# Kernel tuning notes

Measured on AMD Instinct MI355X. Metric: run time of the kernel, lower is better.

Reference implementation:

```python
import jax, jax.numpy as jnp
import numpy as np

K = 8192
D = 512
BETA = 0.25


def setup_inputs() -> dict:
    key = jax.random.key(0)
    k_z, k_cb = jax.random.split(key)
    z = jax.random.normal(k_z, (8, 4096, D), dtype=jnp.float32)
    codebook = jax.random.normal(k_cb, (K, D), dtype=jnp.float32)
    return {"z": z, "codebook": codebook}


def reference(z, codebook):
    B, Q, Din = z.shape
    flat = z.reshape(-1, Din)                      # (N, D)
    x2 = jnp.sum(flat * flat, axis=1, keepdims=True)   # (N, 1)
    e2 = jnp.sum(codebook * codebook, axis=1)          # (K,)
    xe = flat @ codebook.T                             # (N, K)
    distances = x2 - 2.0 * xe + e2[None, :]
    indices = jnp.argmin(distances, axis=1)            # (N,)
    z_q = codebook[indices].reshape(B, Q, Din)

    codebook_loss = jnp.mean((z_q - jax.lax.stop_gradient(z)) ** 2)
    commitment_loss = jnp.mean((z - jax.lax.stop_gradient(z_q)) ** 2)
    vq_loss = codebook_loss + BETA * commitment_loss
    z_q_ste = z + jax.lax.stop_gradient(z_q - z)

    # perplexity from one-hot usage counts of this batch
    N = flat.shape[0]
    counts = jnp.zeros((codebook.shape[0],), dtype=jnp.float32).at[indices].add(1.0)
    probs = counts / jnp.asarray(N, dtype=jnp.float32)
    perplexity = jnp.exp(-jnp.sum(probs * jnp.log(probs + 1e-10)))

    return z_q_ste, vq_loss, indices.reshape(B, Q), perplexity
```

## Files before the change

kernel.cpp:

```cpp
#include <hip/hip_runtime.h>
#include <hip/hip_bf16.h>

#define K_CODES 8192
#define DIM     512
#define N_VEC   32768
#define MARGIN  0.35f

typedef __attribute__((ext_vector_type(8))) short   short8;
typedef __attribute__((ext_vector_type(8))) unsigned short ushort8;
typedef __attribute__((ext_vector_type(4))) float   float4x;

__device__ inline void gl_lds16(const void* g, void* l) {
    __builtin_amdgcn_global_load_lds(
        (const __attribute__((address_space(1))) unsigned int*)g,
        (__attribute__((address_space(3))) unsigned int*)l, 16, 0, 0);
}

__device__ inline unsigned short f2bf(float f) {
    unsigned int u = __float_as_uint(f);
    return (unsigned short)((u + 0x7FFFu + ((u >> 16) & 1u)) >> 16);
}

__global__ __launch_bounds__(256) void vq_prep(
    const float* __restrict__ z, const float* __restrict__ cb,
    float* __restrict__ x2, float* __restrict__ hne2,
    unsigned short* __restrict__ zh, unsigned short* __restrict__ ch) {
    int wave = threadIdx.x >> 6;
    int lane = threadIdx.x & 63;
    int row  = blockIdx.x * 4 + wave;
    bool isZ = row < N_VEC;
    int lr = isZ ? row : row - N_VEC;
    const float* src = isZ ? z + (size_t)row * DIM : cb + (size_t)lr * DIM;

    const float4* s4 = (const float4*)src;
    float4 v0 = s4[lane * 2];
    float4 v1 = s4[lane * 2 + 1];
    float f[8] = {v0.x, v0.y, v0.z, v0.w, v1.x, v1.y, v1.z, v1.w};

    float s = 0.0f;
    ushort8 h8;
#pragma unroll
    for (int i = 0; i < 8; ++i) { s += f[i] * f[i]; h8[i] = f2bf(f[i]); }
    ((ushort8*)(isZ ? zh : ch))[(size_t)lr * 64 + lane] = h8;

#pragma unroll
    for (int off = 32; off >= 1; off >>= 1) s += __shfl_xor(s, off, 64);
    if (lane == 0) {
        if (isZ) x2[lr] = s;
        else     hne2[lr] = -0.5f * s;
    }
}

__global__ __launch_bounds__(256, 2) void vq_gemm(
    const unsigned short* __restrict__ zh, const unsigned short* __restrict__ ch,
    const float* __restrict__ hne2,
    float* __restrict__ pG, int* __restrict__ pN, float* __restrict__ pG2) {
    __shared__ short8 AsC[1024];
    __shared__ short8 BsC[2048];

    const int tid  = threadIdx.x;
    const int w    = tid >> 6;
    const int lane = tid & 63;
    const int wM   = w & 1;
    const int wN   = w >> 1;
    const int rowBase   = blockIdx.x * 128;
    const int half      = blockIdx.y;
    const int codeBase0 = half * 4096;

    const int low3 = lane & 7, m15 = lane & 15, hi4 = lane >> 4;

    unsigned aOff[4];
#pragma unroll
    for (int i = 0; i < 4; ++i) {
        int cell = (w * 4 + i) * 64 + lane;
        int r = cell >> 3, qs = cell & 7, q = qs ^ (r & 7);
        aOff[i] = ((unsigned)(rowBase + r) * DIM + q * 8) * 2;
    }
    unsigned bOff[8];
#pragma unroll
    for (int i = 0; i < 8; ++i) {
        int cell = (w * 8 + i) * 64 + lane;
        int c = cell >> 3, qs = cell & 7, q = qs ^ (c & 7);
        bOff[i] = ((unsigned)c * DIM + q * 8) * 2;
    }

    int rIdx[4], cIdx[8];
#pragma unroll
    for (int mf = 0; mf < 4; ++mf) rIdx[mf] = (wM * 64 + mf * 16 + m15) * 8;
#pragma unroll
    for (int nf = 0; nf < 8; ++nf) cIdx[nf] = (wN * 128 + nf * 16 + m15) * 8;

    float g1[4][4], g2[4][4];
    int   n1[4][4];
#pragma unroll
    for (int mf = 0; mf < 4; ++mf)
#pragma unroll
        for (int rg = 0; rg < 4; ++rg) {
            g1[mf][rg] = -3.4e38f; g2[mf][rg] = -3.4e38f; n1[mf][rg] = 0;
        }

    const char* pA = (const char*)zh;
    for (int ct = 0; ct < 16; ++ct) {
        const int codeBase = codeBase0 + ct * 256;
        const char* pB = (const char*)ch + (size_t)codeBase * (DIM * 2);
        float4x acc[4][8];
#pragma unroll
        for (int mf = 0; mf < 4; ++mf)
#pragma unroll
            for (int nf = 0; nf < 8; ++nf) acc[mf][nf] = (float4x){0.f, 0.f, 0.f, 0.f};

        for (int dc = 0; dc < DIM; dc += 64) {
            const int dc2 = dc * 2;
            __syncthreads();
#pragma unroll
            for (int i = 0; i < 4; ++i)
                gl_lds16(pA + aOff[i] + dc2, &AsC[(w * 4 + i) * 64]);
#pragma unroll
            for (int i = 0; i < 8; ++i)
                gl_lds16(pB + bOff[i] + dc2, &BsC[(w * 8 + i) * 64]);
            __syncthreads();

#pragma unroll
            for (int ks = 0; ks < 2; ++ks) {
                const int qx = (ks * 4 + hi4) ^ low3;
                short8 a[4];
#pragma unroll
                for (int mf = 0; mf < 4; ++mf) a[mf] = AsC[rIdx[mf] + qx];
#pragma unroll
                for (int nf = 0; nf < 8; ++nf) {
                    short8 b = BsC[cIdx[nf] + qx];
#pragma unroll
                    for (int mf = 0; mf < 4; ++mf)
                        acc[mf][nf] = __builtin_amdgcn_mfma_f32_16x16x32_bf16(
                            a[mf], b, acc[mf][nf], 0, 0, 0);
                }
            }
        }

#pragma unroll
        for (int nf = 0; nf < 8; ++nf) {
            int nb = codeBase + wN * 128 + nf * 16 + m15;
            float hv = hne2[nb];
#pragma unroll
            for (int mf = 0; mf < 4; ++mf) {
#pragma unroll
                for (int rg = 0; rg < 4; ++rg) {
                    float g = acc[mf][nf][rg] + hv;
                    if (g > g1[mf][rg]) {
                        g2[mf][rg] = g1[mf][rg];
                        g1[mf][rg] = g; n1[mf][rg] = nb;
                    } else {
                        g2[mf][rg] = fmaxf(g2[mf][rg], g);
                    }
                }
            }
        }
    }

#pragma unroll
    for (int mf = 0; mf < 4; ++mf)
#pragma unroll
        for (int rg = 0; rg < 4; ++rg) {
            float a1 = g1[mf][rg], a2 = g2[mf][rg];
            int   an = n1[mf][rg];
#pragma unroll
            for (int off = 1; off <= 8; off <<= 1) {
                float b1 = __shfl_xor(a1, off, 64);
                int   bn = __shfl_xor(an, off, 64);
                float b2 = __shfl_xor(a2, off, 64);
                if (b1 > a1 || (b1 == a1 && bn < an)) {
                    a2 = fmaxf(a1, b2); a1 = b1; an = bn;
                } else {
                    a2 = fmaxf(a2, b1);
                }
            }
            if (m15 == 0) {
                int row  = rowBase + wM * 64 + mf * 16 + hi4 * 4 + rg;
                int slot = half * 2 + wN;
                pG [slot * N_VEC + row] = a1;
                pN [slot * N_VEC + row] = an;
                pG2[slot * N_VEC + row] = a2;
            }
        }
}

__global__ __launch_bounds__(256) void vq_scan(
    float* __restrict__ pG, const int* __restrict__ pN,
    const float* __restrict__ pG2,
    int* __restrict__ provIdx, int* __restrict__ flags,
    unsigned long long* __restrict__ keys,
    int* __restrict__ rescueRows, int* __restrict__ rescueCnt) {
    int r = blockIdx.x * 256 + threadIdx.x;
    float g1 = pG[r], g2 = pG2[r];
    int   n1 = pN[r];
#pragma unroll
    for (int s = 1; s < 4; ++s) {
        float a1 = pG [s * N_VEC + r];
        int   an = pN [s * N_VEC + r];
        float a2 = pG2[s * N_VEC + r];
        if (a1 > g1 || (a1 == g1 && an < n1)) {
            g2 = fmaxf(g1, a2); g1 = a1; n1 = an;
        } else {
            g2 = fmaxf(g2, a1);
        }
    }
    provIdx[r] = n1;
    pG[r] = g1;
    int fl = (g1 - g2 < MARGIN) ? 1 : 0;
    flags[r] = fl;
    if (fl) {
        keys[r] = ~0ull;
        int p = atomicAdd(rescueCnt, 1);
        rescueRows[p] = r;
    }
}

#define RBM 64
#define RBK 256
#define RBD 32

__global__ __launch_bounds__(256, 2) void vq_rescue(
    const float* __restrict__ z, const float* __restrict__ cb,
    const float* __restrict__ hne2,
    const int* __restrict__ rescueRows, const int* __restrict__ rescueCnt,
    unsigned long long* __restrict__ keys) {
    __shared__ float As[RBD][RBM];
    __shared__ float Bs[RBD][RBK];
    __shared__ int   rowOf[RBM];

    const int tid = threadIdx.x;
    const int tx  = tid & 31;
    const int ty  = tid >> 5;
    const int cnt = *rescueCnt;
    const int codeBase0 = blockIdx.y * 512;
    const int sw = (tx & 8) ? 4 : 0;
    const int sRow = tid >> 2;
    const int sQ   = tid & 3;

    for (int rt = blockIdx.x; rt * RBM < cnt; rt += gridDim.x) {
        const int slotBase = rt * RBM;
        __syncthreads();
        if (tid < RBM) rowOf[tid] = rescueRows[slotBase + tid];
        __syncthreads();

        float best[8];
        int   bidx[8];
#pragma unroll
        for (int i = 0; i < 8; ++i) { best[i] = 3.4e38f; bidx[i] = K_CODES; }

        for (int kt = 0; kt < 2; ++kt) {
            const int codeBase = codeBase0 + kt * RBK;
            float acc[8][8];
#pragma unroll
            for (int i = 0; i < 8; ++i)
#pragma unroll
                for (int j = 0; j < 8; ++j) acc[i][j] = 0.0f;

            for (int dc = 0; dc < DIM; dc += RBD) {
                __syncthreads();
                {
                    const float* srcA = z + (size_t)rowOf[sRow] * DIM + dc + sQ * 8;
                    float4 va0 = ((const float4*)srcA)[0];
                    float4 va1 = ((const float4*)srcA)[1];
                    int c0 = sQ * 8;
                    As[c0 + 0][sRow] = va0.x; As[c0 + 1][sRow] = va0.y;
                    As[c0 + 2][sRow] = va0.z; As[c0 + 3][sRow] = va0.w;
                    As[c0 + 4][sRow] = va1.x; As[c0 + 5][sRow] = va1.y;
                    As[c0 + 6][sRow] = va1.z; As[c0 + 7][sRow] = va1.w;
                }
                {
                    const float4* srcB = (const float4*)(cb + (size_t)(codeBase + tid) * DIM + dc);
#pragma unroll
                    for (int j = 0; j < 8; ++j) {
                        float4 v = srcB[j];
                        Bs[j * 4 + 0][tid] = v.x; Bs[j * 4 + 1][tid] = v.y;
                        Bs[j * 4 + 2][tid] = v.z; Bs[j * 4 + 3][tid] = v.w;
                    }
                }
                __syncthreads();

#pragma unroll
                for (int d = 0; d < RBD; ++d) {
                    float a[8], b[8];
                    *(float4*)&a[0] = *(const float4*)&As[d][ty * 8];
                    *(float4*)&a[4] = *(const float4*)&As[d][ty * 8 + 4];
                    *(float4*)&b[0] = *(const float4*)&Bs[d][tx * 8 + sw];
                    *(float4*)&b[4] = *(const float4*)&Bs[d][tx * 8 + (sw ^ 4)];
#pragma unroll
                    for (int i = 0; i < 8; ++i)
#pragma unroll
                        for (int j = 0; j < 8; ++j) acc[i][j] += a[i] * b[j];
                }
            }

#pragma unroll
            for (int j = 0; j < 8; ++j) {
                int code = codeBase + tx * 8 + ((j < 4) ? (sw + j) : ((sw ^ 4) + j - 4));
                float ev = -hne2[code];
#pragma unroll
                for (int i = 0; i < 8; ++i) {
                    float kv = ev - acc[i][j];
                    if (kv < best[i] || (kv == best[i] && code < bidx[i])) {
                        best[i] = kv;
                        bidx[i] = code;
                    }
                }
            }
        }

#pragma unroll
        for (int off = 16; off >= 1; off >>= 1) {
#pragma unroll
            for (int i = 0; i < 8; ++i) {
                float od = __shfl_xor(best[i], off, 64);
                int   oi = __shfl_xor(bidx[i], off, 64);
                if (od < best[i] || (od == best[i] && oi < bidx[i])) {
                    best[i] = od;
                    bidx[i] = oi;
                }
            }
        }

        if (tx == 0) {
#pragma unroll
            for (int i = 0; i < 8; ++i) {
                int slot = slotBase + ty * 8 + i;
                if (slot < cnt) {
                    unsigned long long key =
                        ((unsigned long long)__float_as_uint(best[i]) << 32) |
                        (unsigned long long)(unsigned)bidx[i];
                    atomicMin(&keys[rowOf[ty * 8 + i]], key);
                }
            }
        }
    }
}

__global__ __launch_bounds__(256) void vq_final(
    const float* __restrict__ gBest, const int* __restrict__ provIdx,
    const int* __restrict__ flags, const unsigned long long* __restrict__ keys,
    const float* __restrict__ x2, const float* __restrict__ cb,
    float* __restrict__ zq, float* __restrict__ idxf,
    float* __restrict__ counts, float* __restrict__ lossAcc) {
    __shared__ int   sIdx[256];
    __shared__ float wsum[4];
    const int tid = threadIdx.x;
    const int r   = blockIdx.x * 256 + tid;

    int n; float dist;
    if (flags[r]) {
        unsigned long long k = keys[r];
        n = (int)(unsigned)(k & 0xffffffffu);
        float kv = __uint_as_float((unsigned)(k >> 32));
        dist = x2[r] + 2.0f * kv;
    } else {
        n = provIdx[r];
        dist = x2[r] - 2.0f * gBest[r];
    }
    sIdx[tid] = n;
    idxf[r]   = (float)n;
    atomicAdd(&counts[n], 1.0f);

    float ls = dist;
#pragma unroll
    for (int off = 32; off >= 1; off >>= 1) ls += __shfl_xor(ls, off, 64);
    if ((tid & 63) == 0) wsum[tid >> 6] = ls;
    __syncthreads();
    if (tid == 0) atomicAdd(lossAcc, wsum[0] + wsum[1] + wsum[2] + wsum[3]);

    const float4* cb4 = (const float4*)cb;
    float4* zq4 = (float4*)(zq + (size_t)blockIdx.x * 256 * DIM);
    for (int t = tid; t < 256 * (DIM / 4); t += 256) {
        int row = t >> 7, f4 = t & 127;
        zq4[(size_t)row * 128 + f4] = cb4[(size_t)sIdx[row] * 128 + f4];
    }
}

__global__ __launch_bounds__(256) void vq_finalize(const float* __restrict__ counts,
                                                   const float* __restrict__ lossAcc,
                                                   float* __restrict__ out_loss,
                                                   float* __restrict__ out_perp) {
    __shared__ float wsum[4];
    int tid = threadIdx.x;
    float s = 0.0f;
    for (int i = tid; i < K_CODES; i += 256) {
        float p = counts[i] * (1.0f / (float)N_VEC);
        s += p * logf(p + 1e-10f);
    }
#pragma unroll
    for (int off = 32; off >= 1; off >>= 1) s += __shfl_xor(s, off, 64);
    if ((tid & 63) == 0) wsum[tid >> 6] = s;
    __syncthreads();
    if (tid == 0) {
        *out_perp = expf(-(wsum[0] + wsum[1] + wsum[2] + wsum[3]));
        *out_loss = 1.25f * lossAcc[0] / (float)(N_VEC * DIM);
    }
}

extern "C" void kernel_launch(void* const* d_in, const int* in_sizes, int n_in,
                              void* d_out, int out_size, void* d_ws, size_t ws_size,
                              hipStream_t stream) {
    (void)in_sizes; (void)n_in; (void)out_size; (void)ws_size;
    const float* z  = (const float*)d_in[0];
    const float* cb = (const float*)d_in[1];

    char* ws = (char*)d_ws;
    float* x2        = (float*)(ws + 0);
    float* hne2      = (float*)(ws + 131072);
    float* counts    = (float*)(ws + 163840);
    float* lossAcc   = (float*)(ws + 196608);
    int*   rescueCnt = (int*)  (ws + 196612);
    int*   provIdx   = (int*)  (ws + 262144);
    int*   flags     = (int*)  (ws + 393216);
    unsigned long long* keys = (unsigned long long*)(ws + 524288);
    int*   rescueRows = (int*) (ws + 786432);
    float* pG        = (float*)(ws + 1048576);
    int*   pN        = (int*)  (ws + 1572864);
    float* pG2       = (float*)(ws + 2097152);
    unsigned short* zh = (unsigned short*)(ws + 2621440);
    unsigned short* ch = (unsigned short*)(ws + 36175872);

    float* out      = (float*)d_out;
    float* zq       = out;
    float* out_loss = out + 16777216;
    float* idxf     = out + 16777217;
    float* out_perp = out + 16777217 + 32768;

    hipMemsetAsync(counts, 0, 32768 + 8, stream);
    hipMemsetAsync(rescueRows, 0, 131072, stream);
    vq_prep<<<(N_VEC + K_CODES) / 4, 256, 0, stream>>>(z, cb, x2, hne2, zh, ch);
    dim3 grid(N_VEC / 128, 2);
    vq_gemm<<<grid, 256, 0, stream>>>(zh, ch, hne2, pG, pN, pG2);
    vq_scan<<<N_VEC / 256, 256, 0, stream>>>(pG, pN, pG2, provIdx, flags, keys,
                                             rescueRows, rescueCnt);
    dim3 rgrid(64, 16);
    vq_rescue<<<rgrid, 256, 0, stream>>>(z, cb, hne2, rescueRows, rescueCnt, keys);
    vq_final<<<N_VEC / 256, 256, 0, stream>>>(pG, provIdx, flags, keys, x2, cb,
                                              zq, idxf, counts, lossAcc);
    vq_finalize<<<1, 256, 0, stream>>>(counts, lossAcc, out_loss, out_perp);
}
```

Measured before the change: 660.4 us.

## Add split-bf16 three-pass MFMA tier between bf16 filter and fp32 rescue

Adds a middle refinement stage. Rows that fall inside the bf16 margin are re-scored with a split-bf16 (hi+lo, three MFMA passes) GEMM against all codes, and a second scan resolves them into keys. Only rows still within a much smaller margin go to the slow fp32 exact kernel, which now runs on a smaller grid. The cost is extra prep work and memory traffic for the low-part arrays, plus two more kernel launches.

```diff
diff --git a/kernel.cpp b/kernel.cpp
--- a/kernel.cpp
+++ b/kernel.cpp
@@ -5,6 +5,7 @@
 #define DIM     512
 #define N_VEC   32768
 #define MARGIN  0.35f
+#define MARGIN2 0.02f
 
 typedef __attribute__((ext_vector_type(8))) short   short8;
 typedef __attribute__((ext_vector_type(8))) unsigned short ushort8;
@@ -16,15 +17,18 @@
         (__attribute__((address_space(3))) unsigned int*)l, 16, 0, 0);
 }
 
-__device__ inline unsigned short f2bf(float f) {
+__device__ inline unsigned short f2bf(float f, float* back) {
     unsigned int u = __float_as_uint(f);
-    return (unsigned short)((u + 0x7FFFu + ((u >> 16) & 1u)) >> 16);
+    unsigned int r = (u + 0x7FFFu + ((u >> 16) & 1u)) >> 16;
+    *back = __uint_as_float(r << 16);
+    return (unsigned short)r;
 }
 
 __global__ __launch_bounds__(256) void vq_prep(
     const float* __restrict__ z, const float* __restrict__ cb,
     float* __restrict__ x2, float* __restrict__ hne2,
-    unsigned short* __restrict__ zh, unsigned short* __restrict__ ch) {
+    unsigned short* __restrict__ zh, unsigned short* __restrict__ zl,
+    unsigned short* __restrict__ ch, unsigned short* __restrict__ cl) {
     int wave = threadIdx.x >> 6;
     int lane = threadIdx.x & 63;
     int row  = blockIdx.x * 4 + wave;
@@ -38,10 +42,16 @@
     float f[8] = {v0.x, v0.y, v0.z, v0.w, v1.x, v1.y, v1.z, v1.w};
 
     float s = 0.0f;
-    ushort8 h8;
-#pragma unroll
-    for (int i = 0; i < 8; ++i) { s += f[i] * f[i]; h8[i] = f2bf(f[i]); }
+    ushort8 h8, l8;
+#pragma unroll
+    for (int i = 0; i < 8; ++i) {
+        s += f[i] * f[i];
+        float back, dummy;
+        h8[i] = f2bf(f[i], &back);
+        l8[i] = f2bf(f[i] - back, &dummy);
+    }
     ((ushort8*)(isZ ? zh : ch))[(size_t)lr * 64 + lane] = h8;
+    ((ushort8*)(isZ ? zl : cl))[(size_t)lr * 64 + lane] = l8;
 
 #pragma unroll
     for (int off = 32; off >= 1; off >>= 1) s += __shfl_xor(s, off, 64);
@@ -215,14 +225,196 @@
     }
 }
 
+__global__ __launch_bounds__(256, 2) void vq_mid(
+    const unsigned short* __restrict__ zh, const unsigned short* __restrict__ zl,
+    const unsigned short* __restrict__ ch, const unsigned short* __restrict__ cl,
+    const float* __restrict__ hne2,
+    const int* __restrict__ rescueRows, const int* __restrict__ rescueCnt,
+    float* __restrict__ pGm, int* __restrict__ pNm, float* __restrict__ pG2m) {
+    __shared__ short8 AsC[512];
+    __shared__ short8 BsC[2048];
+    __shared__ int rowOf[64];
+
+    const int tid  = threadIdx.x;
+    const int w    = tid >> 6;
+    const int lane = tid & 63;
+    const int wM   = w & 1;
+    const int wN   = w >> 1;
+    const int cnt  = *rescueCnt;
+    const int codeBase0 = blockIdx.y * 1024;
+
+    const int low3 = lane & 7, m15 = lane & 15, hi4 = lane >> 4;
+
+    unsigned bOff[8];
+#pragma unroll
+    for (int i = 0; i < 8; ++i) {
+        int cell = (w * 8 + i) * 64 + lane;
+        int c = cell >> 3, qs = cell & 7, q = qs ^ (c & 7);
+        bOff[i] = ((unsigned)c * DIM + q * 8) * 2;
+    }
+    int aCellR[2], aCellQ[2];
+#pragma unroll
+    for (int i = 0; i < 2; ++i) {
+        int cell = (w * 2 + i) * 64 + lane;
+        aCellR[i] = cell >> 3;
+        aCellQ[i] = (cell & 7) ^ (aCellR[i] & 7);
+    }
+
+    int rIdx[2], cIdx[8];
+#pragma unroll
+    for (int mf = 0; mf < 2; ++mf) rIdx[mf] = (wM * 32 + mf * 16 + m15) * 8;
+#pragma unroll
+    for (int nf = 0; nf < 8; ++nf) cIdx[nf] = (wN * 128 + nf * 16 + m15) * 8;
+
+    for (int rt = blockIdx.x; rt * 64 < cnt; rt += gridDim.x) {
+        __syncthreads();
+        if (tid < 64) rowOf[tid] = rescueRows[rt * 64 + tid];
+        __syncthreads();
+
+        unsigned aOff[2];
+#pragma unroll
+        for (int i = 0; i < 2; ++i)
+            aOff[i] = ((unsigned)rowOf[aCellR[i]] * DIM + aCellQ[i] * 8) * 2;
+
+        float g1[2][4], g2[2][4];
+        int   n1[2][4];
+#pragma unroll
+        for (int mf = 0; mf < 2; ++mf)
+#pragma unroll
+            for (int rg = 0; rg < 4; ++rg) {
+                g1[mf][rg] = -3.4e38f; g2[mf][rg] = -3.4e38f; n1[mf][rg] = 0;
+            }
+
+        for (int ct = 0; ct < 4; ++ct) {
+            const int codeBase = codeBase0 + ct * 256;
+            float4x acc[2][8];
+#pragma unroll
+            for (int mf = 0; mf < 2; ++mf)
+#pragma unroll
+                for (int nf = 0; nf < 8; ++nf) acc[mf][nf] = (float4x){0.f, 0.f, 0.f, 0.f};
+
+#pragma unroll
+            for (int pass = 0; pass < 3; ++pass) {
+                const char* pA = (const char*)(pass == 1 ? zl : zh);
+                const char* pB = (const char*)(pass == 2 ? cl : ch)
+                                 + (size_t)codeBase * (DIM * 2);
+                for (int dc = 0; dc < DIM; dc += 64) {
+                    const int dc2 = dc * 2;
+                    __syncthreads();
+#pragma unroll
+                    for (int i = 0; i < 2; ++i)
+                        gl_lds16(pA + aOff[i] + dc2, &AsC[(w * 2 + i) * 64]);
+#pragma unroll
+                    for (int i = 0; i < 8; ++i)
+                        gl_lds16(pB + bOff[i] + dc2, &BsC[(w * 8 + i) * 64]);
+                    __syncthreads();
+
+#pragma unroll
+                    for (int ks = 0; ks < 2; ++ks) {
+                        const int qx = (ks * 4 + hi4) ^ low3;
+                        short8 a[2];
+#pragma unroll
+                        for (int mf = 0; mf < 2; ++mf) a[mf] = AsC[rIdx[mf] + qx];
+#pragma unroll
+                        for (int nf = 0; nf < 8; ++nf) {
+                            short8 b = BsC[cIdx[nf] + qx];
+#pragma unroll
+                            for (int mf = 0; mf < 2; ++mf)
+                                acc[mf][nf] = __builtin_amdgcn_mfma_f32_16x16x32_bf16(
+                                    a[mf], b, acc[mf][nf], 0, 0, 0);
+                        }
+                    }
+                }
+            }
+
+#pragma unroll
+            for (int nf = 0; nf < 8; ++nf) {
+                int nb = codeBase + wN * 128 + nf * 16 + m15;
+                float hv = hne2[nb];
+#pragma unroll
+                for (int mf = 0; mf < 2; ++mf) {
+#pragma unroll
+                    for (int rg = 0; rg < 4; ++rg) {
+                        float g = acc[mf][nf][rg] + hv;
+                        if (g > g1[mf][rg]) {
+                            g2[mf][rg] = g1[mf][rg];
+                            g1[mf][rg] = g; n1[mf][rg] = nb;
+                        } else {
+                            g2[mf][rg] = fmaxf(g2[mf][rg], g);
+                        }
+                    }
+                }
+            }
+        }
+
+#pragma unroll
+        for (int mf = 0; mf < 2; ++mf)
+#pragma unroll
+            for (int rg = 0; rg < 4; ++rg) {
+                float a1 = g1[mf][rg], a2 = g2[mf][rg];
+                int   an = n1[mf][rg];
+#pragma unroll
+                for (int off = 1; off <= 8; off <<= 1) {
+                    float b1 = __shfl_xor(a1, off, 64);
+                    int   bn = __shfl_xor(an, off, 64);
+                    float b2 = __shfl_xor(a2, off, 64);
+                    if (b1 > a1 || (b1 == a1 && bn < an)) {
+                        a2 = fmaxf(a1, b2); a1 = b1; an = bn;
+                    } else {
+                        a2 = fmaxf(a2, b1);
+                    }
+                }
+                if (m15 == 0) {
+                    int sPos = rt * 64 + wM * 32 + mf * 16 + hi4 * 4 + rg;
+                    int slot = blockIdx.y * 2 + wN;
+                    pGm [slot * N_VEC + sPos] = a1;
+                    pNm [slot * N_VEC + sPos] = an;
+                    pG2m[slot * N_VEC + sPos] = a2;
+                }
+            }
+    }
+}
+
+__global__ __launch_bounds__(256) void vq_scan2(
+    const float* __restrict__ pGm, const int* __restrict__ pNm,
+    const float* __restrict__ pG2m,
+    const int* __restrict__ rescueRows, const int* __restrict__ rescueCnt,
+    unsigned long long* __restrict__ keys,
+    int* __restrict__ rescueRows2, int* __restrict__ rescueCnt2) {
+    int s = blockIdx.x * 256 + threadIdx.x;
+    if (s >= *rescueCnt) return;
+    float g1 = pGm[s], g2 = pG2m[s];
+    int   n1 = pNm[s];
+#pragma unroll
+    for (int k = 1; k < 16; ++k) {
+        float a1 = pGm [k * N_VEC + s];
+        int   an = pNm [k * N_VEC + s];
+        float a2 = pG2m[k * N_VEC + s];
+        if (a1 > g1 || (a1 == g1 && an < n1)) {
+            g2 = fmaxf(g1, a2); g1 = a1; n1 = an;
+        } else {
+            g2 = fmaxf(g2, a1);
+        }
+    }
+    int row = rescueRows[s];
+    if (g1 - g2 < MARGIN2) {
+        keys[row] = ~0ull;
+        int p = atomicAdd(rescueCnt2, 1);
+        rescueRows2[p] = row;
+    } else {
+        keys[row] = ((unsigned long long)__float_as_uint(-g1) << 32) |
+                    (unsigned long long)(unsigned)n1;
+    }
+}
+
 #define RBM 64
 #define RBK 256
 #define RBD 32
 
-__global__ __launch_bounds__(256, 2) void vq_rescue(
+__global__ __launch_bounds__(256, 2) void vq_exact(
     const float* __restrict__ z, const float* __restrict__ cb,
     const float* __restrict__ hne2,
-    const int* __restrict__ rescueRows, const int* __restrict__ rescueCnt,
+    const int* __restrict__ rescueRows2, const int* __restrict__ rescueCnt2,
     unsigned long long* __restrict__ keys) {
     __shared__ float As[RBD][RBM];
     __shared__ float Bs[RBD][RBK];
@@ -231,7 +423,7 @@
     const int tid = threadIdx.x;
     const int tx  = tid & 31;
     const int ty  = tid >> 5;
-    const int cnt = *rescueCnt;
+    const int cnt = *rescueCnt2;
     const int codeBase0 = blockIdx.y * 512;
     const int sw = (tx & 8) ? 4 : 0;
     const int sRow = tid >> 2;
@@ -240,7 +432,7 @@
     for (int rt = blockIdx.x; rt * RBM < cnt; rt += gridDim.x) {
         const int slotBase = rt * RBM;
         __syncthreads();
-        if (tid < RBM) rowOf[tid] = rescueRows[slotBase + tid];
+        if (tid < RBM) rowOf[tid] = rescueRows2[slotBase + tid];
         __syncthreads();
 
         float best[8];
@@ -405,20 +597,27 @@
     const float* cb = (const float*)d_in[1];
 
     char* ws = (char*)d_ws;
-    float* x2        = (float*)(ws + 0);
-    float* hne2      = (float*)(ws + 131072);
-    float* counts    = (float*)(ws + 163840);
-    float* lossAcc   = (float*)(ws + 196608);
-    int*   rescueCnt = (int*)  (ws + 196612);
-    int*   provIdx   = (int*)  (ws + 262144);
-    int*   flags     = (int*)  (ws + 393216);
+    float* x2         = (float*)(ws + 0);
+    float* hne2       = (float*)(ws + 131072);
+    float* counts     = (float*)(ws + 163840);
+    float* lossAcc    = (float*)(ws + 196608);
+    int*   rescueCnt  = (int*)  (ws + 196612);
+    int*   rescueCnt2 = (int*)  (ws + 196616);
+    int*   provIdx    = (int*)  (ws + 262144);
+    int*   flags      = (int*)  (ws + 393216);
     unsigned long long* keys = (unsigned long long*)(ws + 524288);
-    int*   rescueRows = (int*) (ws + 786432);
-    float* pG        = (float*)(ws + 1048576);
-    int*   pN        = (int*)  (ws + 1572864);
-    float* pG2       = (float*)(ws + 2097152);
-    unsigned short* zh = (unsigned short*)(ws + 2621440);
-    unsigned short* ch = (unsigned short*)(ws + 36175872);
+    int*   rescueRows  = (int*)(ws + 786432);
+    int*   rescueRows2 = (int*)(ws + 917504);
+    float* pG         = (float*)(ws + 1048576);
+    int*   pN         = (int*)  (ws + 1572864);
+    float* pG2        = (float*)(ws + 2097152);
+    float* pGm        = (float*)(ws + 2621440);
+    int*   pNm        = (int*)  (ws + 4718592);
+    float* pG2m       = (float*)(ws + 6815744);
+    unsigned short* zh = (unsigned short*)(ws + 8912896);
+    unsigned short* zl = (unsigned short*)(ws + 42467328);
+    unsigned short* ch = (unsigned short*)(ws + 76021760);
+    unsigned short* cl = (unsigned short*)(ws + 84410368);
 
     float* out      = (float*)d_out;
     float* zq       = out;
@@ -426,15 +625,20 @@
     float* idxf     = out + 16777217;
     float* out_perp = out + 16777217 + 32768;
 
-    hipMemsetAsync(counts, 0, 32768 + 8, stream);
-    hipMemsetAsync(rescueRows, 0, 131072, stream);
-    vq_prep<<<(N_VEC + K_CODES) / 4, 256, 0, stream>>>(z, cb, x2, hne2, zh, ch);
+    hipMemsetAsync(counts, 0, 32768 + 12, stream);
+    hipMemsetAsync(rescueRows, 0, 262144, stream);
+    vq_prep<<<(N_VEC + K_CODES) / 4, 256, 0, stream>>>(z, cb, x2, hne2, zh, zl, ch, cl);
     dim3 grid(N_VEC / 128, 2);
     vq_gemm<<<grid, 256, 0, stream>>>(zh, ch, hne2, pG, pN, pG2);
     vq_scan<<<N_VEC / 256, 256, 0, stream>>>(pG, pN, pG2, provIdx, flags, keys,
                                              rescueRows, rescueCnt);
-    dim3 rgrid(64, 16);
-    vq_rescue<<<rgrid, 256, 0, stream>>>(z, cb, hne2, rescueRows, rescueCnt, keys);
+    dim3 mgrid(32, 8);
+    vq_mid<<<mgrid, 256, 0, stream>>>(zh, zl, ch, cl, hne2, rescueRows, rescueCnt,
+                                      pGm, pNm, pG2m);
+    vq_scan2<<<N_VEC / 256, 256, 0, stream>>>(pGm, pNm, pG2m, rescueRows, rescueCnt,
+                                              keys, rescueRows2, rescueCnt2);
+    dim3 egrid(8, 16);
+    vq_exact<<<egrid, 256, 0, stream>>>(z, cb, hne2, rescueRows2, rescueCnt2, keys);
     vq_final<<<N_VEC / 256, 256, 0, stream>>>(pG, provIdx, flags, keys, x2, cb,
                                               zq, idxf, counts, lossAcc);
     vq_finalize<<<1, 256, 0, stream>>>(counts, lossAcc, out_loss, out_perp);
```

After: 728.0 us. +10.2%, slower.
